# Kernel tuning notes

Measured on AMD Instinct MI355X. Metric: run time of the kernel, lower is better.

## Reference

```python
import jax, jax.numpy as jnp
import numpy as np

# Production-scale config
N_NODES = 2048      # nodes in input graph
N_UND_EDGES = 4096  # undirected edges (avg degree ~4)
LABELS = 16         # node label categories
FILTERS = 16        # number of learned filter graphs
FNODES = 8          # nodes per filter graph ('nodes' init arg)
HOPS = 3            # egonet radius
MAX_EGO = 128       # egonet padding (covers typical 3-hop size at deg~4)
WL_LEVELS = 4       # initial labels + 3 WL refinements (n_iter=3)


def _mix(h):
    # 32-bit integer hash (lowbias32); equal colors -> equal hash, distinct w.h.p.
    h = h ^ (h >> jnp.uint32(16))
    h = h * jnp.uint32(0x7FEB352D)
    h = h ^ (h >> jnp.uint32(15))
    h = h * jnp.uint32(0x846CA68B)
    h = h ^ (h >> jnp.uint32(16))
    return h


def _wl_step(adj_u32, h):
    # multiset-hash WL relabel: new color = hash(old color, sum of hashed neighbor colors)
    msg = jnp.einsum('guv,gv->gu', adj_u32, _mix(h))  # uint32 wraparound sum
    return _mix(h * jnp.uint32(0x9E3779B1) + msg)


def _max_cc_mask(B):
    # largest connected component of a small binary graph via min-label propagation
    M = B.shape[0]
    lbl = jnp.arange(M)
    Bb = B > 0
    for _ in range(M):
        nb = jnp.min(jnp.where(Bb, lbl[None, :], M), axis=1)
        lbl = jnp.minimum(lbl, nb)
    cnt = (lbl[:, None] == lbl[None, :]).sum(1)
    return lbl == lbl[jnp.argmax(cnt)]


def setup_inputs() -> dict:
    key = jax.random.key(0)
    k1, k2, k3, k4, k5 = jax.random.split(key, 5)
    x = jax.random.normal(k1, (N_NODES, LABELS), dtype=jnp.float32)
    src = jax.random.randint(k2, (N_UND_EDGES,), 0, N_NODES)
    dst = jax.random.randint(k3, (N_UND_EDGES,), 0, N_NODES)
    edge_index = jnp.stack([jnp.concatenate([src, dst]),
                            jnp.concatenate([dst, src])]).astype(jnp.int32)
    batch = jnp.zeros((N_NODES,), dtype=jnp.int32)
    # filter adjacency exactly as in GKernel.__init__: symmetric binarized, zero diag
    Ar = jax.random.uniform(k4, (FILTERS, FNODES, FNODES))
    A = ((Ar + jnp.swapaxes(Ar, -2, -1)) > 1.0).astype(jnp.float32)
    A = A * (1.0 - jnp.eye(FNODES, dtype=jnp.float32))
    X = 10.0 * jax.random.normal(k5, (FILTERS, FNODES, LABELS), dtype=jnp.float32)
    return {"x": x, "edge_index": edge_index, "batch": batch, "A": A, "X": X}


def reference(x, edge_index, batch, A, X):
    N = x.shape[0]
    F, M = A.shape[0], A.shape[1]
    # dense symmetric adjacency of the input graph
    Adense = jnp.zeros((N, N), jnp.float32).at[edge_index[0], edge_index[1]].set(1.0)
    Adense = jnp.maximum(Adense, Adense.T)
    # 3-hop reachability (egonet membership), seed always included
    r = jnp.eye(N, dtype=jnp.float32)
    for _ in range(HOPS):
        r = ((r + r @ Adense) > 0).astype(jnp.float32)
    reach = r > 0
    ar = jnp.arange(N)
    # pick up to MAX_EGO member nodes per egonet (seed forced first)
    scores = reach.astype(jnp.int32) * (2 * N) - ar[None, :]
    scores = scores + jnp.where(ar[None, :] == ar[:, None], 8 * N, 0)
    _, idx = jax.lax.top_k(scores, MAX_EGO)                 # [N, K]
    emask = jnp.take_along_axis(reach, idx, axis=1).astype(jnp.float32)  # [N, K]
    adj_ego = Adense[idx[:, :, None], idx[:, None, :]] * emask[:, :, None] * emask[:, None, :]
    lab_e = jnp.argmax(x, -1)[idx]                          # [N, K] initial WL labels
    # filter graphs: keep only largest connected component (max_comp)
    fmask = jax.vmap(_max_cc_mask)(A).astype(jnp.float32)   # [F, M]
    Bf = A * fmask[:, :, None] * fmask[:, None, :]
    lab_f = jnp.argmax(X, -1)                               # [F, M]
    # WL color refinement + vertex-histogram kernel accumulation
    adj_e_u = adj_ego.astype(jnp.uint32)
    adj_f_u = Bf.astype(jnp.uint32)
    h_e = _mix(lab_e.astype(jnp.uint32) + jnp.uint32(1))
    h_f = _mix(lab_f.astype(jnp.uint32) + jnp.uint32(1))
    cross = jnp.zeros((N, F), jnp.float32)
    self_e = jnp.zeros((N,), jnp.float32)
    self_f = jnp.zeros((F,), jnp.float32)
    for t in range(WL_LEVELS):
        if t > 0:
            h_e = _wl_step(adj_e_u, h_e)
            h_f = _wl_step(adj_f_u, h_f)
        hf_flat = h_f.reshape(-1)                           # [F*M]
        eq = (h_e[:, :, None] == hf_flat[None, None, :]).astype(jnp.float32)  # [N,K,F*M]
        s = (eq * emask[:, :, None]).sum(1).reshape(N, F, M)
        cross = cross + (s * fmask[None]).sum(-1)
        eqee = (h_e[:, :, None] == h_e[:, None, :]).astype(jnp.float32)       # [N,K,K]
        self_e = self_e + (eqee * emask[:, :, None] * emask[:, None, :]).sum((1, 2))
        eqff = (h_f[:, :, None] == h_f[:, None, :]).astype(jnp.float32)       # [F,M,M]
        self_f = self_f + (eqff * fmask[:, :, None] * fmask[:, None, :]).sum((1, 2))
    sim = cross / jnp.sqrt(self_e[:, None] * self_f[None, :])  # normalized WL kernel
    return jnp.nan_to_num(sim)                              # [N, FILTERS]
```

## Files before the change

kernel.cpp:

```cpp
#include <hip/hip_runtime.h>
#include <hip/hip_bf16.h>
#include <stdint.h>

#define N_NODES 2048
#define WORDS   32
#define LABELS  16
#define FILTERS 16
#define FNODES  8
#define MAX_EGO 128
#define WL_LEVELS 4
#define IDCAP   256

typedef unsigned long long u64;

__device__ __forceinline__ unsigned mixu(unsigned h) {
    h ^= h >> 16; h *= 0x7FEB352Du;
    h ^= h >> 15; h *= 0x846CA68Bu;
    h ^= h >> 16;
    return h;
}

__global__ void __launch_bounds__(64)
build_adj_kernel(const int* __restrict__ ei, int E2, u64* __restrict__ Adense,
                 const float* __restrict__ Af, const float* __restrict__ Xf,
                 unsigned* __restrict__ hfg, unsigned* __restrict__ fmbg,
                 float* __restrict__ selfg) {
    const int lane = threadIdx.x;
    if ((int)blockIdx.x < (int)gridDim.x - 1) {
        int e = blockIdx.x * 64 + lane;
        if (e < E2) {
            int s = ei[e], d = ei[E2 + e];
            atomicOr(&Adense[(size_t)s * WORDS + (d >> 6)], 1ull << (d & 63));
            atomicOr(&Adense[(size_t)d * WORDS + (s >> 6)], 1ull << (s & 63));
        }
        return;
    }
    if (lane >= FILTERS) return;
    int f = lane;
    const float* Aff = Af + (size_t)f * FNODES * FNODES;
    unsigned row[FNODES];
    for (int m = 0; m < FNODES; ++m) {
        unsigned r = 0;
        for (int j = 0; j < FNODES; ++j)
            if (Aff[m * FNODES + j] > 0.f) r |= 1u << j;
        row[m] = r;
    }
    const float* Xff = Xf + (size_t)f * FNODES * LABELS;
    unsigned lab[FNODES];
    for (int m = 0; m < FNODES; ++m) {
        const float* xr = Xff + m * LABELS;
        float best = xr[0]; int bi = 0;
        for (int c = 1; c < LABELS; ++c) { float v = xr[c]; if (v > best) { best = v; bi = c; } }
        lab[m] = (unsigned)(bi + 1);
    }
    int lbl[FNODES];
    for (int m = 0; m < FNODES; ++m) lbl[m] = m;
    for (int it = 0; it < FNODES; ++it) {
        int nb2[FNODES];
        for (int m = 0; m < FNODES; ++m) {
            int mn = FNODES;
            for (int j = 0; j < FNODES; ++j)
                if ((row[m] >> j) & 1) mn = min(mn, lbl[j]);
            nb2[m] = mn;
        }
        for (int m = 0; m < FNODES; ++m) lbl[m] = min(lbl[m], nb2[m]);
    }
    int cnt[FNODES];
    for (int m = 0; m < FNODES; ++m) {
        int c = 0;
        for (int j = 0; j < FNODES; ++j) c += (lbl[j] == lbl[m]);
        cnt[m] = c;
    }
    int best = 0;
    for (int m = 1; m < FNODES; ++m) if (cnt[m] > cnt[best]) best = m;
    unsigned fm = 0;
    for (int m = 0; m < FNODES; ++m) if (lbl[m] == lbl[best]) fm |= 1u << m;
    fmbg[f] = fm;
    unsigned brow[FNODES];
    for (int m = 0; m < FNODES; ++m) brow[m] = ((fm >> m) & 1) ? (row[m] & fm) : 0u;
    unsigned hh[FNODES];
    for (int m = 0; m < FNODES; ++m) hh[m] = mixu(lab[m]);
    float sf = 0.f;
    for (int t = 0; t < WL_LEVELS; ++t) {
        if (t > 0) {
            unsigned mx[FNODES], nh[FNODES];
            for (int m = 0; m < FNODES; ++m) mx[m] = mixu(hh[m]);
            for (int m = 0; m < FNODES; ++m) {
                unsigned msg = 0;
                for (int j = 0; j < FNODES; ++j)
                    if ((brow[m] >> j) & 1) msg += mx[j];
                nh[m] = mixu(hh[m] * 0x9E3779B1u + msg);
            }
            for (int m = 0; m < FNODES; ++m) hh[m] = nh[m];
        }
        for (int m = 0; m < FNODES; ++m)
            hfg[t * FILTERS * FNODES + f * FNODES + m] = hh[m];
        int c = 0;
        for (int m = 0; m < FNODES; ++m) if ((fm >> m) & 1)
            for (int j = 0; j < FNODES; ++j) if ((fm >> j) & 1) c += (hh[m] == hh[j]);
        sf += (float)c;
    }
    selfg[f] = sf;
}

__global__ void __launch_bounds__(64)
ego_kernel(const float* __restrict__ x,
           const u64* __restrict__ Adense,
           const unsigned* __restrict__ hfg, const unsigned* __restrict__ fmbg,
           const float* __restrict__ selfg, float* __restrict__ out) {
    const int i    = blockIdx.x;
    const int lane = threadIdx.x;
    const int w    = lane & 31;
    const int hwp  = lane >> 5;

    __shared__ u64 arow[WORDS];
    __shared__ u64 r2s[WORDS];
    __shared__ u64 mmask[WORDS];
    __shared__ unsigned pfx[WORDS];
    __shared__ unsigned idlist[IDCAP];
    __shared__ unsigned members[MAX_EGO];
    __shared__ __align__(16) unsigned h[MAX_EGO];
    __shared__ unsigned msgacc[MAX_EGO];
    __shared__ __align__(16) unsigned adjs[MAX_EGO][4];
    __shared__ unsigned hf_s[WL_LEVELS * FILTERS * FNODES];
    __shared__ unsigned fmb[FILTERS];
    __shared__ float    selff_s[FILTERS];
    __shared__ unsigned cross_sh[FILTERS];
    __shared__ unsigned selfe_sh;

    for (int t = lane; t < WL_LEVELS * FILTERS * FNODES; t += 64) hf_s[t] = hfg[t];
    if (lane < FILTERS) { fmb[lane] = fmbg[lane]; selff_s[lane] = selfg[lane]; }
    #pragma unroll
    for (int t = lane; t < MAX_EGO * 4; t += 64) ((unsigned*)adjs)[t] = 0;
    if (lane < WORDS) arow[lane] = Adense[(size_t)i * WORDS + lane];
    __syncthreads();

    int n1;
    {
        u64 v = arow[w];
        int pc = __popcll(v);
        int incl = pc;
        for (int d = 1; d < 32; d <<= 1) {
            int t2 = __shfl_up(incl, d, 32);
            if (w >= d) incl += t2;
        }
        int ex = incl - pc;
        u64 vv = v; int r = 0;
        while (vv) {
            int b = __ffsll(vv) - 1; vv &= vv - 1;
            if (ex + r < IDCAP) idlist[ex + r] = (unsigned)((w << 6) + b);
            ++r;
        }
        n1 = min(__shfl(incl, 31, 32), IDCAP);
    }
    __syncthreads();

    u64 racc = arow[w];
    if ((i >> 6) == w) racc |= 1ull << (i & 63);
    for (int t = hwp; t < n1; t += 16) {
        u64 vb[8];
        #pragma unroll
        for (int k = 0; k < 8; ++k) {
            int tk = t + 2 * k;
            vb[k] = (tk < n1) ? Adense[(size_t)idlist[tk] * WORDS + w] : 0ull;
        }
        racc |= vb[0] | vb[1] | vb[2] | vb[3] | vb[4] | vb[5] | vb[6] | vb[7];
    }
    racc |= __shfl_xor(racc, 32, 64);
    r2s[w] = racc;
    __syncthreads();

    int n2;
    {
        u64 v = r2s[w];
        int pc = __popcll(v);
        int incl = pc;
        for (int d = 1; d < 32; d <<= 1) {
            int t2 = __shfl_up(incl, d, 32);
            if (w >= d) incl += t2;
        }
        int ex = incl - pc;
        u64 vv = v; int r = 0;
        while (vv) {
            int b = __ffsll(vv) - 1; vv &= vv - 1;
            if (ex + r < IDCAP) idlist[ex + r] = (unsigned)((w << 6) + b);
            ++r;
        }
        n2 = min(__shfl(incl, 31, 32), IDCAP);
    }
    __syncthreads();

    u64 acc3 = racc;
    for (int t = hwp; t < n2; t += 16) {
        u64 vb[8];
        #pragma unroll
        for (int k = 0; k < 8; ++k) {
            int tk = t + 2 * k;
            vb[k] = (tk < n2) ? Adense[(size_t)idlist[tk] * WORDS + w] : 0ull;
        }
        acc3 |= vb[0] | vb[1] | vb[2] | vb[3] | vb[4] | vb[5] | vb[6] | vb[7];
    }
    acc3 |= __shfl_xor(acc3, 32, 64);

    int S;
    {
        u64 v = acc3;
        int seedw = i >> 6;
        u64 seedbit = 1ull << (i & 63);
        if (w == seedw) v &= ~seedbit;
        int pc = __popcll(v);
        int incl = pc;
        for (int d = 1; d < 32; d <<= 1) {
            int t2 = __shfl_up(incl, d, 32);
            if (w >= d) incl += t2;
        }
        int excl = incl - pc;
        const int keep = MAX_EGO - 1;
        if (excl >= keep) {
            v = 0;
        } else {
            int allow = keep - excl;
            while (pc > allow) {
                v &= ~(1ull << (63 - __clzll(v)));
                --pc;
            }
        }
        if (w == seedw) v |= seedbit;
        mmask[w] = v;
        int pc2 = __popcll(v);
        int incl2 = pc2;
        for (int d = 1; d < 32; d <<= 1) {
            int t2 = __shfl_up(incl2, d, 32);
            if (w >= d) incl2 += t2;
        }
        int ex2 = incl2 - pc2;
        pfx[w] = (unsigned)ex2;
        u64 vv = v;
        int r = 0;
        while (vv) {
            int b = __ffsll(vv) - 1;
            vv &= vv - 1;
            members[ex2 + r] = (unsigned)((w << 6) + b);
            ++r;
        }
        S = __shfl(incl2, 31, 32);
    }
    __syncthreads();
    const int s0 = lane, s1 = lane + 64;
    const bool p0 = (s0 < S), p1 = (s1 < S);

    unsigned hv0 = 0, hv1 = 0;
    {
        if (p0) {
            const float4* xr = (const float4*)(x + (size_t)members[s0] * LABELS);
            float4 a0 = xr[0], a1 = xr[1], a2 = xr[2], a3 = xr[3];
            float vv[16] = {a0.x,a0.y,a0.z,a0.w,a1.x,a1.y,a1.z,a1.w,
                            a2.x,a2.y,a2.z,a2.w,a3.x,a3.y,a3.z,a3.w};
            float best = vv[0]; int bi = 0;
            #pragma unroll
            for (int c = 1; c < 16; ++c) { if (vv[c] > best) { best = vv[c]; bi = c; } }
            hv0 = mixu((unsigned)(bi + 1));
            h[s0] = hv0;
        }
        if (p1) {
            const float4* xr = (const float4*)(x + (size_t)members[s1] * LABELS);
            float4 a0 = xr[0], a1 = xr[1], a2 = xr[2], a3 = xr[3];
            float vv[16] = {a0.x,a0.y,a0.z,a0.w,a1.x,a1.y,a1.z,a1.w,
                            a2.x,a2.y,a2.z,a2.w,a3.x,a3.y,a3.z,a3.w};
            float best = vv[0]; int bi = 0;
            #pragma unroll
            for (int c = 1; c < 16; ++c) { if (vv[c] > best) { best = vv[c]; bi = c; } }
            hv1 = mixu((unsigned)(bi + 1));
            h[s1] = hv1;
        }
    }

    {
        const u64 mw = mmask[w];
        const unsigned base = pfx[w];
        for (int t = hwp; t < S; t += 16) {
            u64 vb[8];
            int ti[8];
            #pragma unroll
            for (int k = 0; k < 8; ++k) {
                ti[k] = t + 2 * k;
                vb[k] = (ti[k] < S) ? (Adense[(size_t)members[ti[k]] * WORDS + w] & mw) : 0ull;
            }
            #pragma unroll
            for (int k = 0; k < 8; ++k) {
                u64 v = vb[k];
                while (v) {
                    int b = __ffsll(v) - 1; v &= v - 1;
                    int slot = (int)base + __popcll(mw & ((1ull << b) - 1));
                    atomicOr(&adjs[ti[k]][slot >> 5], 1u << (slot & 31));
                }
            }
        }
    }
    __syncthreads();

    uint4 aw0 = *(const uint4*)adjs[s0];
    uint4 aw1 = *(const uint4*)adjs[s1];

    unsigned crossReg[FILTERS];
    #pragma unroll
    for (int f = 0; f < FILTERS; ++f) crossReg[f] = 0;
    unsigned selfeReg = 0;

    for (int t = 0; t < WL_LEVELS; ++t) {
        if (t > 0) {
            msgacc[lane] = 0u; msgacc[lane + 64] = 0u;
            __syncthreads();
            if (p0) {
                unsigned mixv = mixu(hv0);
                unsigned bw[4] = {aw0.x, aw0.y, aw0.z, aw0.w};
                #pragma unroll
                for (int ww = 0; ww < 4; ++ww) {
                    unsigned bits = bw[ww];
                    while (bits) { int l = __ffs(bits) - 1; bits &= bits - 1;
                                   atomicAdd(&msgacc[(ww << 5) + l], mixv); }
                }
            }
            if (p1) {
                unsigned mixv = mixu(hv1);
                unsigned bw[4] = {aw1.x, aw1.y, aw1.z, aw1.w};
                #pragma unroll
                for (int ww = 0; ww < 4; ++ww) {
                    unsigned bits = bw[ww];
                    while (bits) { int l = __ffs(bits) - 1; bits &= bits - 1;
                                   atomicAdd(&msgacc[(ww << 5) + l], mixv); }
                }
            }
            __syncthreads();
            if (p0) { hv0 = mixu(hv0 * 0x9E3779B1u + msgacc[s0]); h[s0] = hv0; }
            if (p1) { hv1 = mixu(hv1 * 0x9E3779B1u + msgacc[s1]); h[s1] = hv1; }
            __syncthreads();
        }

        const unsigned* hrow = &hf_s[t * FILTERS * FNODES];
        if (p0) {
            #pragma unroll
            for (int f = 0; f < FILTERS; ++f) {
                unsigned fm = fmb[f], c = 0;
                #pragma unroll
                for (int m = 0; m < FNODES; ++m)
                    c += (unsigned)((hv0 == hrow[f * FNODES + m]) & ((fm >> m) & 1u));
                crossReg[f] += c;
            }
        }
        if (p1) {
            #pragma unroll
            for (int f = 0; f < FILTERS; ++f) {
                unsigned fm = fmb[f], c = 0;
                #pragma unroll
                for (int m = 0; m < FNODES; ++m)
                    c += (unsigned)((hv1 == hrow[f * FNODES + m]) & ((fm >> m) & 1u));
                crossReg[f] += c;
            }
        }
        {
            unsigned ce = 0;
            const int quads = S >> 2;
            const uint4* h4 = (const uint4*)h;
            for (int qq = 0; qq < quads; ++qq) {
                uint4 hh = h4[qq];
                if (p0) ce += (unsigned)(hh.x == hv0) + (unsigned)(hh.y == hv0)
                            + (unsigned)(hh.z == hv0) + (unsigned)(hh.w == hv0);
                if (p1) ce += (unsigned)(hh.x == hv1) + (unsigned)(hh.y == hv1)
                            + (unsigned)(hh.z == hv1) + (unsigned)(hh.w == hv1);
            }
            for (int l = quads << 2; l < S; ++l) {
                unsigned hl = h[l];
                if (p0) ce += (unsigned)(hl == hv0);
                if (p1) ce += (unsigned)(hl == hv1);
            }
            selfeReg += ce;
        }
        __syncthreads();
    }

    #pragma unroll
    for (int f = 0; f < FILTERS; ++f) {
        unsigned v = crossReg[f];
        for (int o = 32; o > 0; o >>= 1) v += __shfl_down(v, o, 64);
        crossReg[f] = v;
    }
    {
        unsigned v = selfeReg;
        for (int o = 32; o > 0; o >>= 1) v += __shfl_down(v, o, 64);
        selfeReg = v;
    }
    if (lane == 0) {
        #pragma unroll
        for (int f = 0; f < FILTERS; ++f) cross_sh[f] = crossReg[f];
        selfe_sh = selfeReg;
    }
    __syncthreads();
    if (lane < FILTERS) {
        float se = (float)selfe_sh;
        float sf = selff_s[lane];
        float denom = sqrtf(se * sf);
        float v = (denom > 0.f) ? ((float)cross_sh[lane] / denom) : 0.f;
        out[(size_t)i * FILTERS + lane] = v;
    }
}

extern "C" void kernel_launch(void* const* d_in, const int* in_sizes, int n_in,
                              void* d_out, int out_size, void* d_ws, size_t ws_size,
                              hipStream_t stream) {
    const float* x  = (const float*)d_in[0];
    const int*   ei = (const int*)d_in[1];
    const float* A  = (const float*)d_in[3];
    const float* X  = (const float*)d_in[4];
    float* out = (float*)d_out;
    int E2 = in_sizes[1] / 2;

    char* ws = (char*)d_ws;
    const size_t ADJ_BYTES = (size_t)N_NODES * WORDS * sizeof(u64);
    u64* Adense = (u64*)(ws);
    unsigned* hfg    = (unsigned*)(ws + ADJ_BYTES);
    unsigned* fmbg   = (unsigned*)(ws + ADJ_BYTES + 4096);
    float*    selfg  = (float*)  (ws + ADJ_BYTES + 4096 + 256);

    hipMemsetAsync(Adense, 0, ADJ_BYTES, stream);
    int nbE = (E2 + 63) / 64;
    build_adj_kernel<<<nbE + 1, 64, 0, stream>>>(ei, E2, Adense, A, X, hfg, fmbg, selfg);
    ego_kernel<<<N_NODES, 64, 0, stream>>>(x, Adense, hfg, fmbg, selfg, out);
}
```

Measured before the change: 130.7 us.

## Replace per-filter hash comparisons with global hash table of packed filter counts

Filter WL colors are inserted into a per-level open-addressing hash table keyed by hash value. Each slot holds per-filter match counts packed as bytes in two 64-bit words. Each ego node now does one table probe per level instead of 128 compares against shared-memory filter hashes. Cross counts are kept as packed 64-bit accumulators and unpacked before the reduction. The changes risk a key that hashes to zero being treated as an empty slot, and byte overflow if counts exceed 255 per lane.

```diff
diff --git a/kernel.cpp b/kernel.cpp
--- a/kernel.cpp
+++ b/kernel.cpp
@@ -10,6 +10,7 @@
 #define MAX_EGO 128
 #define WL_LEVELS 4
 #define IDCAP   256
+#define TSLOTS  256
 
 typedef unsigned long long u64;
 
@@ -23,8 +24,8 @@
 __global__ void __launch_bounds__(64)
 build_adj_kernel(const int* __restrict__ ei, int E2, u64* __restrict__ Adense,
                  const float* __restrict__ Af, const float* __restrict__ Xf,
-                 unsigned* __restrict__ hfg, unsigned* __restrict__ fmbg,
-                 float* __restrict__ selfg) {
+                 unsigned* __restrict__ tkeys, u64* __restrict__ tval0,
+                 u64* __restrict__ tval1, float* __restrict__ selfg) {
     const int lane = threadIdx.x;
     if ((int)blockIdx.x < (int)gridDim.x - 1) {
         int e = blockIdx.x * 64 + lane;
@@ -75,7 +76,6 @@
     for (int m = 1; m < FNODES; ++m) if (cnt[m] > cnt[best]) best = m;
     unsigned fm = 0;
     for (int m = 0; m < FNODES; ++m) if (lbl[m] == lbl[best]) fm |= 1u << m;
-    fmbg[f] = fm;
     unsigned brow[FNODES];
     for (int m = 0; m < FNODES; ++m) brow[m] = ((fm >> m) & 1) ? (row[m] & fm) : 0u;
     unsigned hh[FNODES];
@@ -93,8 +93,18 @@
             }
             for (int m = 0; m < FNODES; ++m) hh[m] = nh[m];
         }
-        for (int m = 0; m < FNODES; ++m)
-            hfg[t * FILTERS * FNODES + f * FNODES + m] = hh[m];
+        for (int m = 0; m < FNODES; ++m) {
+            if (!((fm >> m) & 1)) continue;
+            unsigned key = hh[m];
+            int p = (int)(key & (TSLOTS - 1));
+            for (;;) {
+                unsigned old = atomicCAS(&tkeys[t * TSLOTS + p], 0u, key);
+                if (old == 0u || old == key) break;
+                p = (p + 1) & (TSLOTS - 1);
+            }
+            if (f < 8) atomicAdd(&tval0[t * TSLOTS + p], 1ull << (8 * f));
+            else       atomicAdd(&tval1[t * TSLOTS + p], 1ull << (8 * (f - 8)));
+        }
         int c = 0;
         for (int m = 0; m < FNODES; ++m) if ((fm >> m) & 1)
             for (int j = 0; j < FNODES; ++j) if ((fm >> j) & 1) c += (hh[m] == hh[j]);
@@ -106,7 +116,8 @@
 __global__ void __launch_bounds__(64)
 ego_kernel(const float* __restrict__ x,
            const u64* __restrict__ Adense,
-           const unsigned* __restrict__ hfg, const unsigned* __restrict__ fmbg,
+           const unsigned* __restrict__ tkeys, const u64* __restrict__ tval0,
+           const u64* __restrict__ tval1,
            const float* __restrict__ selfg, float* __restrict__ out) {
     const int i    = blockIdx.x;
     const int lane = threadIdx.x;
@@ -122,14 +133,11 @@
     __shared__ __align__(16) unsigned h[MAX_EGO];
     __shared__ unsigned msgacc[MAX_EGO];
     __shared__ __align__(16) unsigned adjs[MAX_EGO][4];
-    __shared__ unsigned hf_s[WL_LEVELS * FILTERS * FNODES];
-    __shared__ unsigned fmb[FILTERS];
     __shared__ float    selff_s[FILTERS];
     __shared__ unsigned cross_sh[FILTERS];
     __shared__ unsigned selfe_sh;
 
-    for (int t = lane; t < WL_LEVELS * FILTERS * FNODES; t += 64) hf_s[t] = hfg[t];
-    if (lane < FILTERS) { fmb[lane] = fmbg[lane]; selff_s[lane] = selfg[lane]; }
+    if (lane < FILTERS) selff_s[lane] = selfg[lane];
     #pragma unroll
     for (int t = lane; t < MAX_EGO * 4; t += 64) ((unsigned*)adjs)[t] = 0;
     if (lane < WORDS) arow[lane] = Adense[(size_t)i * WORDS + lane];
@@ -302,9 +310,7 @@
     uint4 aw0 = *(const uint4*)adjs[s0];
     uint4 aw1 = *(const uint4*)adjs[s1];
 
-    unsigned crossReg[FILTERS];
-    #pragma unroll
-    for (int f = 0; f < FILTERS; ++f) crossReg[f] = 0;
+    u64 accA = 0, accB = 0;
     unsigned selfeReg = 0;
 
     for (int t = 0; t < WL_LEVELS; ++t) {
@@ -337,27 +343,20 @@
             __syncthreads();
         }
 
-        const unsigned* hrow = &hf_s[t * FILTERS * FNODES];
+        const unsigned* tk = tkeys + t * TSLOTS;
         if (p0) {
-            #pragma unroll
-            for (int f = 0; f < FILTERS; ++f) {
-                unsigned fm = fmb[f], c = 0;
-                #pragma unroll
-                for (int m = 0; m < FNODES; ++m)
-                    c += (unsigned)((hv0 == hrow[f * FNODES + m]) & ((fm >> m) & 1u));
-                crossReg[f] += c;
-            }
+            int p = (int)(hv0 & (TSLOTS - 1));
+            unsigned k;
+            while ((k = tk[p]) != 0u && k != hv0) p = (p + 1) & (TSLOTS - 1);
+            if (k == hv0) { accA += tval0[t * TSLOTS + p]; accB += tval1[t * TSLOTS + p]; }
         }
         if (p1) {
-            #pragma unroll
-            for (int f = 0; f < FILTERS; ++f) {
-                unsigned fm = fmb[f], c = 0;
-                #pragma unroll
-                for (int m = 0; m < FNODES; ++m)
-                    c += (unsigned)((hv1 == hrow[f * FNODES + m]) & ((fm >> m) & 1u));
-                crossReg[f] += c;
-            }
-        }
+            int p = (int)(hv1 & (TSLOTS - 1));
+            unsigned k;
+            while ((k = tk[p]) != 0u && k != hv1) p = (p + 1) & (TSLOTS - 1);
+            if (k == hv1) { accA += tval0[t * TSLOTS + p]; accB += tval1[t * TSLOTS + p]; }
+        }
+
         {
             unsigned ce = 0;
             const int quads = S >> 2;
@@ -379,6 +378,12 @@
         __syncthreads();
     }
 
+    unsigned crossReg[FILTERS];
+    #pragma unroll
+    for (int k = 0; k < 8; ++k) {
+        crossReg[k]     = (unsigned)((accA >> (8 * k)) & 0xFFull);
+        crossReg[k + 8] = (unsigned)((accB >> (8 * k)) & 0xFFull);
+    }
     #pragma unroll
     for (int f = 0; f < FILTERS; ++f) {
         unsigned v = crossReg[f];
@@ -418,12 +423,14 @@
     char* ws = (char*)d_ws;
     const size_t ADJ_BYTES = (size_t)N_NODES * WORDS * sizeof(u64);
     u64* Adense = (u64*)(ws);
-    unsigned* hfg    = (unsigned*)(ws + ADJ_BYTES);
-    unsigned* fmbg   = (unsigned*)(ws + ADJ_BYTES + 4096);
-    float*    selfg  = (float*)  (ws + ADJ_BYTES + 4096 + 256);
-
-    hipMemsetAsync(Adense, 0, ADJ_BYTES, stream);
+    unsigned* tkeys = (unsigned*)(ws + ADJ_BYTES);
+    u64*      tval0 = (u64*)     (ws + ADJ_BYTES + 4096);
+    u64*      tval1 = (u64*)     (ws + ADJ_BYTES + 4096 + 8192);
+    float*    selfg = (float*)   (ws + ADJ_BYTES + 4096 + 16384);
+
+    hipMemsetAsync(Adense, 0, ADJ_BYTES + 4096 + 16384, stream);
     int nbE = (E2 + 63) / 64;
-    build_adj_kernel<<<nbE + 1, 64, 0, stream>>>(ei, E2, Adense, A, X, hfg, fmbg, selfg);
-    ego_kernel<<<N_NODES, 64, 0, stream>>>(x, Adense, hfg, fmbg, selfg, out);
+    build_adj_kernel<<<nbE + 1, 64, 0, stream>>>(ei, E2, Adense, A, X,
+                                                 tkeys, tval0, tval1, selfg);
+    ego_kernel<<<N_NODES, 64, 0, stream>>>(x, Adense, tkeys, tval0, tval1, selfg, out);
 }
```

New measurement: 152.0 us. 16.3% more time.
